# Performance work log

Measured on AMD Instinct MI355X. Metric: run time of the kernel, lower is better.

## Reference

```python
import jax, jax.numpy as jnp
import numpy as np

NUM_HEADS = 12


def setup_inputs() -> dict:
    key = jax.random.key(0)
    ks = jax.random.split(key, 20)
    T, B, D = 1024, 8, 768
    s = 1.0 / np.sqrt(D)
    inp = {
        "query": jax.random.normal(ks[0], (T, B, D), jnp.float32),
        "key": jax.random.normal(ks[1], (T, B, D), jnp.float32),
        "value": jax.random.normal(ks[2], (T, B, D), jnp.float32),
        "ls_len": 512,
    }
    names = ["Wq", "Wk", "Wv", "Wqm", "Wkm", "Wvm", "Wo"]
    for i, n in enumerate(names):
        inp[n] = jax.random.normal(ks[3 + i], (D, D), jnp.float32) * s
        inp["b" + n[1:]] = jnp.zeros((D,), jnp.float32)
    return inp


def reference(query, key, value, ls_len, Wq, bq, Wk, bk, Wv, bv,
              Wqm, bqm, Wkm, bkm, Wvm, bvm, Wo, bo):
    T, B, D = query.shape
    H = NUM_HEADS
    hd = D // H
    scaling = float(hd) ** -0.5

    def proj(x, W, b):
        return x @ W.T + b

    # modal-split projections along the sequence (dim 0), then re-concat
    q = jnp.concatenate([proj(query[:ls_len], Wq, bq),
                         proj(query[ls_len:], Wqm, bqm)], axis=0) * scaling
    k = jnp.concatenate([proj(key[:ls_len], Wk, bk),
                         proj(key[ls_len:], Wkm, bkm)], axis=0)
    v = jnp.concatenate([proj(value[:ls_len], Wv, bv),
                         proj(value[ls_len:], Wvm, bvm)], axis=0)

    # (T, B, D) -> (B*H, T, hd)
    def to_heads(x):
        return x.reshape(x.shape[0], B * H, hd).transpose(1, 0, 2)

    q, k, v = to_heads(q), to_heads(k), to_heads(v)
    scores = jnp.einsum("bth,bsh->bts", q, k)        # (B*H, T, S)
    attn = jax.nn.softmax(scores, axis=-1)
    out = jnp.einsum("bts,bsh->bth", attn, v)        # (B*H, T, hd)
    out = out.transpose(1, 0, 2).reshape(T, B, D)
    return out @ Wo.T + bo
```

## Files before the change

kernel.cpp:

```cpp
#include <hip/hip_runtime.h>

#define T_  1024
#define B_  8
#define D_  768
#define H_  12
#define HD_ 64
#define BH_ 96
#define M_  8192
#define XSZ 6291456ull
#define WSZ 589824ull

typedef __attribute__((ext_vector_type(8))) short short8;
typedef __attribute__((ext_vector_type(4))) float f32x4;

__device__ __forceinline__ unsigned short f2bf(float f) {
    unsigned int u = __float_as_uint(f);
    u += 0x7FFF + ((u >> 16) & 1);
    return (unsigned short)(u >> 16);
}

__device__ __forceinline__ void g2lds16(const unsigned short* g, unsigned short* l) {
    __builtin_amdgcn_global_load_lds(
        (const __attribute__((address_space(1))) unsigned int*)(g),
        (__attribute__((address_space(3))) unsigned int*)(l),
        16, 0, 0);
}

__global__ __launch_bounds__(256)
void convert_kernel(const float* __restrict__ q, const float* __restrict__ k,
                    const float* __restrict__ v,
                    const float* __restrict__ wq, const float* __restrict__ wk,
                    const float* __restrict__ wv, const float* __restrict__ wqm,
                    const float* __restrict__ wkm, const float* __restrict__ wvm,
                    const float* __restrict__ wo,
                    unsigned short* __restrict__ dst)
{
    const int seg = blockIdx.y;
    const float* s; size_t off, n;
    switch (seg) {
        case 0: s = q;   off = 0;               n = XSZ; break;
        case 1: s = k;   off = XSZ;             n = XSZ; break;
        case 2: s = v;   off = 2*XSZ;           n = XSZ; break;
        case 3: s = wq;  off = 3*XSZ;           n = WSZ; break;
        case 4: s = wk;  off = 3*XSZ +   WSZ;   n = WSZ; break;
        case 5: s = wv;  off = 3*XSZ + 2*WSZ;   n = WSZ; break;
        case 6: s = wqm; off = 3*XSZ + 3*WSZ;   n = WSZ; break;
        case 7: s = wkm; off = 3*XSZ + 4*WSZ;   n = WSZ; break;
        case 8: s = wvm; off = 3*XSZ + 5*WSZ;   n = WSZ; break;
        default:s = wo;  off = 3*XSZ + 6*WSZ;   n = WSZ; break;
    }
    unsigned short* d = dst + off;
    const size_t stride = (size_t)gridDim.x * blockDim.x;
    for (size_t i = (size_t)blockIdx.x * blockDim.x + threadIdx.x; i < n / 4; i += stride) {
        const float4 f = reinterpret_cast<const float4*>(s)[i];
        ushort4 o;
        o.x = f2bf(f.x); o.y = f2bf(f.y); o.z = f2bf(f.z); o.w = f2bf(f.w);
        reinterpret_cast<ushort4*>(d)[i] = o;
    }
}

__device__ __forceinline__ void stage_tile(const unsigned short* __restrict__ A,
                                           const unsigned short* __restrict__ B,
                                           int m0, int n0, int ks,
                                           unsigned short* lds, int buf, int tid)
{
    const int w = tid >> 6, l = tid & 63;
    const int rsub = l >> 2;
    const int cg   = (l & 3) ^ ((l >> 3) & 3);
    const int koff = ks * 32 + cg * 8;
    #pragma unroll
    for (int p = 0; p < 2; ++p) {
        const int rbase = p * 128 + w * 16;
        g2lds16(&A[(size_t)(m0 + rbase + rsub) * D_ + koff],
                &lds[buf * 12288 + rbase * 32]);
    }
    {
        const int rbase = w * 16;
        g2lds16(&B[(size_t)(n0 + rbase + rsub) * D_ + koff],
                &lds[buf * 12288 + 8192 + rbase * 32]);
    }
}

__device__ __forceinline__ void mfma_step(const unsigned short* lds, int buf,
                                          int wr, int wc, int lr, int lg,
                                          f32x4 acc[4][4])
{
    const int slot = (lg ^ ((lr >> 1) & 3)) * 8;
    short8 a[4], b[4];
    #pragma unroll
    for (int m = 0; m < 4; ++m)
        a[m] = *reinterpret_cast<const short8*>(
            &lds[buf * 12288 + (wr * 64 + 16 * m + lr) * 32 + slot]);
    #pragma unroll
    for (int n = 0; n < 4; ++n)
        b[n] = *reinterpret_cast<const short8*>(
            &lds[buf * 12288 + 8192 + (wc * 64 + 16 * n + lr) * 32 + slot]);
    #pragma unroll
    for (int m = 0; m < 4; ++m)
        #pragma unroll
        for (int n = 0; n < 4; ++n)
            acc[m][n] = __builtin_amdgcn_mfma_f32_16x16x32_bf16(a[m], b[n], acc[m][n], 0, 0, 0);
}

#define GEMM_CORE(Aptr, Bptr)                                                  \
    f32x4 acc[4][4];                                                           \
    _Pragma("unroll") for (int m = 0; m < 4; ++m)                              \
        _Pragma("unroll") for (int n = 0; n < 4; ++n)                          \
            acc[m][n] = (f32x4){0.f, 0.f, 0.f, 0.f};                           \
    stage_tile(Aptr, Bptr, m0, n0, 0, lds, 0, tid);                            \
    __syncthreads();                                                           \
    for (int ks = 0; ks < 24; ++ks) {                                          \
        if (ks < 23) stage_tile(Aptr, Bptr, m0, n0, ks + 1, lds, (ks + 1) & 1, tid); \
        mfma_step(lds, ks & 1, wr, wc, lr, lg, acc);                           \
        __syncthreads();                                                       \
    }

__global__ __launch_bounds__(512)
void qkv_gemm(const unsigned short* __restrict__ xb,
              const unsigned short* __restrict__ wb,
              const int* __restrict__ ls_ptr,
              const float* __restrict__ bq,  const float* __restrict__ bk,
              const float* __restrict__ bv,  const float* __restrict__ bqm,
              const float* __restrict__ bkm, const float* __restrict__ bvm,
              unsigned short* __restrict__ qh, unsigned short* __restrict__ kh,
              unsigned short* __restrict__ vt)
{
    __shared__ unsigned short lds[24576];
    const int bid = blockIdx.x;
    const int L   = (bid & 7) * 72 + (bid >> 3);
    const int z   = L / 192;
    const int rem = L - z * 192;
    const int mi  = rem / 6;
    const int ni  = rem - mi * 6;
    const int m0 = mi * 256, n0 = ni * 128;

    const int tid = threadIdx.x;
    const int w = tid >> 6, l = tid & 63, lr = l & 15, lg = l >> 4;
    const int wr = w >> 1, wc = w & 1;

    const bool modal = (m0 >= ls_ptr[0] * B_);
    const unsigned short* A = xb + (size_t)z * XSZ;
    const unsigned short* W = wb + (size_t)(z + (modal ? 3 : 0)) * WSZ;
    const float* bias = modal ? (z == 0 ? bqm : z == 1 ? bkm : bvm)
                              : (z == 0 ? bq  : z == 1 ? bk  : bv);

    GEMM_CORE(A, W)

    float bn[4];
    #pragma unroll
    for (int n = 0; n < 4; ++n) bn[n] = bias[n0 + wc * 64 + 16 * n + lr];

    if (z < 2) {
        unsigned short* dst = (z == 0) ? qh : kh;
        const float scale = (z == 0) ? 0.18033688011112042f : 1.0f;
        #pragma unroll
        for (int m = 0; m < 4; ++m) {
            const int grb = m0 + wr * 64 + 16 * m + 4 * lg;
            #pragma unroll
            for (int n = 0; n < 4; ++n) {
                const int gc = n0 + wc * 64 + 16 * n + lr;
                const int h = gc >> 6, e = gc & 63;
                #pragma unroll
                for (int j = 0; j < 4; ++j) {
                    const int gr = grb + j, t = gr >> 3, b = gr & 7;
                    dst[((size_t)(b * H_ + h) * T_ + t) * HD_ + e] =
                        f2bf((acc[m][n][j] + bn[n]) * scale);
                }
            }
        }
    } else {
        #pragma unroll
        for (int m = 0; m < 4; ++m) {
            const int grb = m0 + wr * 64 + 16 * m + 4 * lg;
            #pragma unroll
            for (int n = 0; n < 4; ++n) {
                const int gc = n0 + wc * 64 + 16 * n + lr;
                const int h = gc >> 6, e = gc & 63;
                #pragma unroll
                for (int j = 0; j < 4; ++j) {
                    const int gr = grb + j, t = gr >> 3, b = gr & 7;
                    vt[((size_t)(b * H_ + h) * HD_ + e) * T_ + t] =
                        f2bf(acc[m][n][j] + bn[n]);
                }
            }
        }
    }
}

__global__ __launch_bounds__(512)
void out_gemm(const unsigned short* __restrict__ aob,
              const unsigned short* __restrict__ wo,
              const float* __restrict__ bo, float* __restrict__ out)
{
    __shared__ unsigned short lds[24576];
    const int bid = blockIdx.x;
    const int L   = (bid & 7) * 24 + (bid >> 3);
    const int mi  = L / 6, ni = L - mi * 6;
    const int m0 = mi * 256, n0 = ni * 128;

    const int tid = threadIdx.x;
    const int w = tid >> 6, l = tid & 63, lr = l & 15, lg = l >> 4;
    const int wr = w >> 1, wc = w & 1;

    GEMM_CORE(aob, wo)

    float bn[4];
    #pragma unroll
    for (int n = 0; n < 4; ++n) bn[n] = bo[n0 + wc * 64 + 16 * n + lr];

    #pragma unroll
    for (int m = 0; m < 4; ++m) {
        const int grb = m0 + wr * 64 + 16 * m + 4 * lg;
        #pragma unroll
        for (int n = 0; n < 4; ++n) {
            const int gc = n0 + wc * 64 + 16 * n + lr;
            #pragma unroll
            for (int j = 0; j < 4; ++j) {
                const int gr = grb + j;
                out[(size_t)gr * D_ + gc] = acc[m][n][j] + bn[n];
            }
        }
    }
}

__device__ __forceinline__ void stage_kv(const unsigned short* __restrict__ khh,
                                         const unsigned short* __restrict__ vth,
                                         int kt, unsigned short* KsB,
                                         unsigned short* VtB, int w, int l)
{
    const int rbase = w * 8;
    const int row   = rbase + (l >> 3);
    const int cg    = (l & 7) ^ ((l >> 3) & 7);
    g2lds16(&khh[(size_t)(kt * 64 + row) * HD_ + cg * 8], &KsB[rbase * 64]);
    g2lds16(&vth[(size_t)row * T_ + kt * 64 + cg * 8],    &VtB[rbase * 64]);
}

__global__ __launch_bounds__(512)
void attn_kernel_bf16(const unsigned short* __restrict__ qh,
                      const unsigned short* __restrict__ kh,
                      const unsigned short* __restrict__ vt,
                      unsigned short* __restrict__ aob)
{
    const int bid = blockIdx.x;
    const int L   = (bid & 7) * 96 + (bid >> 3);
    const int bh  = L >> 3;
    const int qt  = L & 7;

    const int tid = threadIdx.x;
    const int w   = tid >> 6;
    const int l   = tid & 63;
    const int lr  = l & 15;
    const int lg  = l >> 4;

    __shared__ unsigned short Ks[2][4096];
    __shared__ unsigned short Vt[2][4096];
    __shared__ unsigned short Ps[8192];

    const unsigned short* khh = kh + (size_t)bh * T_ * HD_;
    const unsigned short* vth = vt + (size_t)bh * HD_ * T_;
    const size_t qk_head = (size_t)bh * T_ * HD_;

    short8 qf[2];
    #pragma unroll
    for (int c = 0; c < 2; ++c)
        qf[c] = *reinterpret_cast<const short8*>(
            &qh[qk_head + (size_t)(qt * 128 + 16 * w + lr) * HD_ + 8 * lg + 32 * c]);

    const short one_bf = (short)0x3F80;
    const short8 ones8 = {one_bf, one_bf, one_bf, one_bf,
                          one_bf, one_bf, one_bf, one_bf};

    f32x4 o[4];
    #pragma unroll
    for (int ef = 0; ef < 4; ++ef) o[ef] = (f32x4){0.f, 0.f, 0.f, 0.f};
    f32x4 lsumf = (f32x4){0.f, 0.f, 0.f, 0.f};

    stage_kv(khh, vth, 0, Ks[0], Vt[0], w, l);
    asm volatile("s_waitcnt vmcnt(0)" ::: "memory");
    __builtin_amdgcn_s_barrier();

    int buf = 0;
    for (int kt = 0; kt < 16; ++kt) {
        __builtin_amdgcn_sched_barrier(0);
        if (kt < 15)
            stage_kv(khh, vth, kt + 1, Ks[buf ^ 1], Vt[buf ^ 1], w, l);

        f32x4 s[4];
        #pragma unroll
        for (int nf = 0; nf < 4; ++nf) s[nf] = (f32x4){0.f, 0.f, 0.f, 0.f};
        #pragma unroll
        for (int c = 0; c < 2; ++c) {
            #pragma unroll
            for (int nf = 0; nf < 4; ++nf) {
                const short8 kb = *reinterpret_cast<const short8*>(
                    &Ks[buf][(16 * nf + lr) * 64 + ((8 * lg + 32 * c) ^ ((lr & 7) << 3))]);
                s[nf] = __builtin_amdgcn_mfma_f32_16x16x32_bf16(qf[c], kb, s[nf], 0, 0, 0);
            }
        }

        #pragma unroll
        for (int r = 0; r < 4; ++r) {
            const int q  = 16 * w + 4 * lg + r;
            const int qx = ((4 * lg + r) & 7) << 3;
            #pragma unroll
            for (int nf = 0; nf < 4; ++nf)
                Ps[q * 64 + ((16 * nf + lr) ^ qx)] =
                    f2bf(exp2f(s[nf][r] - 16.0f));
        }
        asm volatile("s_waitcnt lgkmcnt(0)" ::: "memory");
        __builtin_amdgcn_sched_barrier(0);
        __builtin_amdgcn_s_barrier();
        __builtin_amdgcn_sched_barrier(0);

        const int prow = 16 * w + lr;
        #pragma unroll
        for (int c = 0; c < 2; ++c) {
            const short8 pa = *reinterpret_cast<const short8*>(
                &Ps[prow * 64 + ((8 * lg + 32 * c) ^ ((prow & 7) << 3))]);
            #pragma unroll
            for (int ef = 0; ef < 4; ++ef) {
                const short8 vb = *reinterpret_cast<const short8*>(
                    &Vt[buf][(16 * ef + lr) * 64 + ((8 * lg + 32 * c) ^ ((lr & 7) << 3))]);
                o[ef] = __builtin_amdgcn_mfma_f32_16x16x32_bf16(pa, vb, o[ef], 0, 0, 0);
            }
            lsumf = __builtin_amdgcn_mfma_f32_16x16x32_bf16(pa, ones8, lsumf, 0, 0, 0);
        }

        asm volatile("s_waitcnt vmcnt(0) lgkmcnt(0)" ::: "memory");
        __builtin_amdgcn_sched_barrier(0);
        __builtin_amdgcn_s_barrier();
        __builtin_amdgcn_sched_barrier(0);
        buf ^= 1;
    }

    const int b = bh / H_, h = bh % H_;
    #pragma unroll
    for (int r = 0; r < 4; ++r) {
        const int t = qt * 128 + 16 * w + 4 * lg + r;
        const float inv = 1.0f / lsumf[r];
        #pragma unroll
        for (int ef = 0; ef < 4; ++ef)
            aob[((size_t)t * B_ + b) * D_ + h * HD_ + 16 * ef + lr] =
                f2bf(o[ef][r] * inv);
    }
}

extern "C" void kernel_launch(void* const* d_in, const int* in_sizes, int n_in,
                              void* d_out, int out_size, void* d_ws, size_t ws_size,
                              hipStream_t stream)
{
    const float* query = (const float*)d_in[0];
    const float* keyi  = (const float*)d_in[1];
    const float* value = (const float*)d_in[2];
    const int*   lsp   = (const int*)  d_in[3];
    const float* Wq  = (const float*)d_in[4],  *bq  = (const float*)d_in[5];
    const float* Wk  = (const float*)d_in[6],  *bk  = (const float*)d_in[7];
    const float* Wv  = (const float*)d_in[8],  *bv  = (const float*)d_in[9];
    const float* Wqm = (const float*)d_in[10], *bqm = (const float*)d_in[11];
    const float* Wkm = (const float*)d_in[12], *bkm = (const float*)d_in[13];
    const float* Wvm = (const float*)d_in[14], *bvm = (const float*)d_in[15];
    const float* Wo  = (const float*)d_in[16], *bo  = (const float*)d_in[17];

    unsigned short* ws = (unsigned short*)d_ws;
    unsigned short* xb  = ws;
    unsigned short* wb  = xb + 3 * XSZ;
    unsigned short* qh  = wb + 7 * WSZ;
    unsigned short* kh  = qh + XSZ;
    unsigned short* vt  = kh + XSZ;
    unsigned short* aob = vt + XSZ;

    dim3 gc_(512, 10);
    convert_kernel<<<gc_, 256, 0, stream>>>(query, keyi, value,
                                            Wq, Wk, Wv, Wqm, Wkm, Wvm, Wo, xb);

    qkv_gemm<<<576, 512, 0, stream>>>(xb, wb, lsp, bq, bk, bv, bqm, bkm, bvm,
                                      qh, kh, vt);

    attn_kernel_bf16<<<768, 512, 0, stream>>>(qh, kh, vt, aob);

    out_gemm<<<192, 512, 0, stream>>>(aob, wb + 6 * WSZ, bo, (float*)d_out);
}
```

Measured before the change: 186.7 us.

## Use 256x256x64 GEMM tiles with a two-stage prefetch pipeline and explicit waitcnts

Widens the projection and output GEMM tiles from 256x128 with k-step 32 to 256x256 with k-step 64, using a wider XOR swizzle and 8x4 accumulators per wave. Loads are issued two stages ahead, and the syncthreads barriers are replaced by explicit vmcnt/lgkmcnt waits around raw barriers. This is meant to raise arithmetic intensity and cut the number of barriers. In exchange the block count halves (288 and 96 blocks, so the output GEMM fills fewer CUs than the MI355X has), LDS use grows to 128KB per block, and register pressure is higher.

```diff
diff --git a/kernel.cpp b/kernel.cpp
--- a/kernel.cpp
+++ b/kernel.cpp
@@ -59,60 +59,68 @@
     }
 }
 
-__device__ __forceinline__ void stage_tile(const unsigned short* __restrict__ A,
-                                           const unsigned short* __restrict__ B,
-                                           int m0, int n0, int ks,
-                                           unsigned short* lds, int buf, int tid)
+__device__ __forceinline__ void stage256(const unsigned short* __restrict__ A,
+                                         const unsigned short* __restrict__ B,
+                                         int m0, int n0, int ks,
+                                         unsigned short* lds, int buf, int tid)
 {
     const int w = tid >> 6, l = tid & 63;
-    const int rsub = l >> 2;
-    const int cg   = (l & 3) ^ ((l >> 3) & 3);
-    const int koff = ks * 32 + cg * 8;
-    #pragma unroll
-    for (int p = 0; p < 2; ++p) {
-        const int rbase = p * 128 + w * 16;
+    const int rsub = l >> 3;
+    const int cg   = (l & 7) ^ rsub;
+    const int koff = ks * 64 + cg * 8;
+    #pragma unroll
+    for (int p = 0; p < 4; ++p) {
+        const int rbase = p * 64 + w * 8;
         g2lds16(&A[(size_t)(m0 + rbase + rsub) * D_ + koff],
-                &lds[buf * 12288 + rbase * 32]);
-    }
-    {
-        const int rbase = w * 16;
+                &lds[buf * 32768 + rbase * 64]);
         g2lds16(&B[(size_t)(n0 + rbase + rsub) * D_ + koff],
-                &lds[buf * 12288 + 8192 + rbase * 32]);
-    }
-}
-
-__device__ __forceinline__ void mfma_step(const unsigned short* lds, int buf,
-                                          int wr, int wc, int lr, int lg,
-                                          f32x4 acc[4][4])
-{
-    const int slot = (lg ^ ((lr >> 1) & 3)) * 8;
-    short8 a[4], b[4];
-    #pragma unroll
-    for (int m = 0; m < 4; ++m)
-        a[m] = *reinterpret_cast<const short8*>(
-            &lds[buf * 12288 + (wr * 64 + 16 * m + lr) * 32 + slot]);
-    #pragma unroll
-    for (int n = 0; n < 4; ++n)
-        b[n] = *reinterpret_cast<const short8*>(
-            &lds[buf * 12288 + 8192 + (wc * 64 + 16 * n + lr) * 32 + slot]);
-    #pragma unroll
-    for (int m = 0; m < 4; ++m)
+                &lds[buf * 32768 + 16384 + rbase * 64]);
+    }
+}
+
+__device__ __forceinline__ void mfma256(const unsigned short* lds, int buf,
+                                        int wr, int wc, int lr, int lg,
+                                        f32x4 acc[8][4])
+{
+    #pragma unroll
+    for (int kk = 0; kk < 2; ++kk) {
+        const int slot = ((kk * 4 + lg) ^ (lr & 7)) * 8;
+        short8 a[8], b[4];
+        #pragma unroll
+        for (int m = 0; m < 8; ++m)
+            a[m] = *reinterpret_cast<const short8*>(
+                &lds[buf * 32768 + (wr * 128 + 16 * m + lr) * 64 + slot]);
         #pragma unroll
         for (int n = 0; n < 4; ++n)
-            acc[m][n] = __builtin_amdgcn_mfma_f32_16x16x32_bf16(a[m], b[n], acc[m][n], 0, 0, 0);
-}
-
-#define GEMM_CORE(Aptr, Bptr)                                                  \
-    f32x4 acc[4][4];                                                           \
-    _Pragma("unroll") for (int m = 0; m < 4; ++m)                              \
+            b[n] = *reinterpret_cast<const short8*>(
+                &lds[buf * 32768 + 16384 + (wc * 64 + 16 * n + lr) * 64 + slot]);
+        #pragma unroll
+        for (int m = 0; m < 8; ++m)
+            #pragma unroll
+            for (int n = 0; n < 4; ++n)
+                acc[m][n] = __builtin_amdgcn_mfma_f32_16x16x32_bf16(a[m], b[n], acc[m][n], 0, 0, 0);
+    }
+}
+
+#define GEMM256_CORE(Aptr, Bptr)                                               \
+    f32x4 acc[8][4];                                                           \
+    _Pragma("unroll") for (int m = 0; m < 8; ++m)                              \
         _Pragma("unroll") for (int n = 0; n < 4; ++n)                          \
             acc[m][n] = (f32x4){0.f, 0.f, 0.f, 0.f};                           \
-    stage_tile(Aptr, Bptr, m0, n0, 0, lds, 0, tid);                            \
-    __syncthreads();                                                           \
-    for (int ks = 0; ks < 24; ++ks) {                                          \
-        if (ks < 23) stage_tile(Aptr, Bptr, m0, n0, ks + 1, lds, (ks + 1) & 1, tid); \
-        mfma_step(lds, ks & 1, wr, wc, lr, lg, acc);                           \
-        __syncthreads();                                                       \
+    stage256(Aptr, Bptr, m0, n0, 0, lds, 0, tid);                              \
+    stage256(Aptr, Bptr, m0, n0, 1, lds, 1, tid);                              \
+    for (int t = 0; t < 12; ++t) {                                             \
+        if (t < 11) { asm volatile("s_waitcnt vmcnt(8) lgkmcnt(0)" ::: "memory"); } \
+        else        { asm volatile("s_waitcnt vmcnt(0) lgkmcnt(0)" ::: "memory"); } \
+        __builtin_amdgcn_sched_barrier(0);                                     \
+        __builtin_amdgcn_s_barrier();                                          \
+        __builtin_amdgcn_sched_barrier(0);                                     \
+        mfma256(lds, t & 1, wr, wc, lr, lg, acc);                              \
+        asm volatile("s_waitcnt lgkmcnt(0)" ::: "memory");                     \
+        __builtin_amdgcn_sched_barrier(0);                                     \
+        __builtin_amdgcn_s_barrier();                                          \
+        __builtin_amdgcn_sched_barrier(0);                                     \
+        if (t < 10) stage256(Aptr, Bptr, m0, n0, t + 2, lds, t & 1, tid);      \
     }
 
 __global__ __launch_bounds__(512)
@@ -125,18 +133,18 @@
               unsigned short* __restrict__ qh, unsigned short* __restrict__ kh,
               unsigned short* __restrict__ vt)
 {
-    __shared__ unsigned short lds[24576];
+    __shared__ unsigned short lds[65536];
     const int bid = blockIdx.x;
-    const int L   = (bid & 7) * 72 + (bid >> 3);
-    const int z   = L / 192;
-    const int rem = L - z * 192;
-    const int mi  = rem / 6;
-    const int ni  = rem - mi * 6;
-    const int m0 = mi * 256, n0 = ni * 128;
+    const int L   = (bid & 7) * 36 + (bid >> 3);
+    const int z   = L / 96;
+    const int rem = L - z * 96;
+    const int mi  = rem / 3;
+    const int ni  = rem - mi * 3;
+    const int m0 = mi * 256, n0 = ni * 256;
 
     const int tid = threadIdx.x;
     const int w = tid >> 6, l = tid & 63, lr = l & 15, lg = l >> 4;
-    const int wr = w >> 1, wc = w & 1;
+    const int wr = w >> 2, wc = w & 3;
 
     const bool modal = (m0 >= ls_ptr[0] * B_);
     const unsigned short* A = xb + (size_t)z * XSZ;
@@ -144,7 +152,7 @@
     const float* bias = modal ? (z == 0 ? bqm : z == 1 ? bkm : bvm)
                               : (z == 0 ? bq  : z == 1 ? bk  : bv);
 
-    GEMM_CORE(A, W)
+    GEMM256_CORE(A, W)
 
     float bn[4];
     #pragma unroll
@@ -154,8 +162,8 @@
         unsigned short* dst = (z == 0) ? qh : kh;
         const float scale = (z == 0) ? 0.18033688011112042f : 1.0f;
         #pragma unroll
-        for (int m = 0; m < 4; ++m) {
-            const int grb = m0 + wr * 64 + 16 * m + 4 * lg;
+        for (int m = 0; m < 8; ++m) {
+            const int grb = m0 + wr * 128 + 16 * m + 4 * lg;
             #pragma unroll
             for (int n = 0; n < 4; ++n) {
                 const int gc = n0 + wc * 64 + 16 * n + lr;
@@ -170,8 +178,8 @@
         }
     } else {
         #pragma unroll
-        for (int m = 0; m < 4; ++m) {
-            const int grb = m0 + wr * 64 + 16 * m + 4 * lg;
+        for (int m = 0; m < 8; ++m) {
+            const int grb = m0 + wr * 128 + 16 * m + 4 * lg;
             #pragma unroll
             for (int n = 0; n < 4; ++n) {
                 const int gc = n0 + wc * 64 + 16 * n + lr;
@@ -192,25 +200,25 @@
               const unsigned short* __restrict__ wo,
               const float* __restrict__ bo, float* __restrict__ out)
 {
-    __shared__ unsigned short lds[24576];
+    __shared__ unsigned short lds[65536];
     const int bid = blockIdx.x;
-    const int L   = (bid & 7) * 24 + (bid >> 3);
-    const int mi  = L / 6, ni = L - mi * 6;
-    const int m0 = mi * 256, n0 = ni * 128;
+    const int L   = (bid & 7) * 12 + (bid >> 3);
+    const int mi  = L / 3, ni = L - mi * 3;
+    const int m0 = mi * 256, n0 = ni * 256;
 
     const int tid = threadIdx.x;
     const int w = tid >> 6, l = tid & 63, lr = l & 15, lg = l >> 4;
-    const int wr = w >> 1, wc = w & 1;
-
-    GEMM_CORE(aob, wo)
+    const int wr = w >> 2, wc = w & 3;
+
+    GEMM256_CORE(aob, wo)
 
     float bn[4];
     #pragma unroll
     for (int n = 0; n < 4; ++n) bn[n] = bo[n0 + wc * 64 + 16 * n + lr];
 
     #pragma unroll
-    for (int m = 0; m < 4; ++m) {
-        const int grb = m0 + wr * 64 + 16 * m + 4 * lg;
+    for (int m = 0; m < 8; ++m) {
+        const int grb = m0 + wr * 128 + 16 * m + 4 * lg;
         #pragma unroll
         for (int n = 0; n < 4; ++n) {
             const int gc = n0 + wc * 64 + 16 * n + lr;
@@ -373,10 +381,10 @@
     convert_kernel<<<gc_, 256, 0, stream>>>(query, keyi, value,
                                             Wq, Wk, Wv, Wqm, Wkm, Wvm, Wo, xb);
 
-    qkv_gemm<<<576, 512, 0, stream>>>(xb, wb, lsp, bq, bk, bv, bqm, bkm, bvm,
+    qkv_gemm<<<288, 512, 0, stream>>>(xb, wb, lsp, bq, bk, bv, bqm, bkm, bvm,
                                       qh, kh, vt);
 
     attn_kernel_bf16<<<768, 512, 0, stream>>>(qh, kh, vt, aob);
 
-    out_gemm<<<192, 512, 0, stream>>>(aob, wb + 6 * WSZ, bo, (float*)d_out);
-}
+    out_gemm<<<96, 512, 0, stream>>>(aob, wb + 6 * WSZ, bo, (float*)d_out);
+}
```

Measured after the change: 254.0 us. +36.0%, slower.
